# Kernel optimization log

Hardware: AMD Instinct MI355X
Metric: run time of the kernel (lower is better)

The kernel has to match this reference:

```python
import jax, jax.numpy as jnp
import numpy as np


def setup_inputs() -> dict:
    key = jax.random.key(0)
    k1, k2, k3 = jax.random.split(key, 3)
    B, H, L, D = 4, 16, 1024, 64
    q = jax.random.normal(k1, (B, H, L, D), dtype=jnp.float32)
    k = jax.random.normal(k2, (B, H, L, D), dtype=jnp.float32)
    attn_mask = jax.random.randint(k3, (B, H, L, L), 0, 2).astype(bool)
    return {"q": q, "k": k, "attn_mask": attn_mask}


def reference(q, k, attn_mask):
    # q, k: [B, H, L, D]. The original builds a [B,H,L,D,L] tensor
    # c[b,h,i,m,j] = exp(-(q[b,h,i,m]-k[b,h,j,m])^2), then for each dim m
    # keeps only the entries where rank of q[i,m] (along seq) equals rank of
    # k[j,m], scatters them into an LxL grid and averages over m.
    # Equivalent fused form: sort q and k per dimension, pair equal ranks,
    # and scatter-add exp(-(q_sorted - k_sorted)^2)/D into p[b,h,i,j].
    B, H, L, D = q.shape
    q_idx = jnp.argsort(q, axis=2)                       # [B,H,L,D] int
    k_idx = jnp.argsort(k, axis=2)
    q_sorted = jnp.take_along_axis(q, q_idx, axis=2)     # [B,H,L,D]
    k_sorted = jnp.take_along_axis(k, k_idx, axis=2)
    diff = q_sorted - k_sorted
    vals = jnp.exp(-(diff * diff))                       # [B,H,L,D]
    # linear index into the flattened [L,L] grid, plus batch*head offset
    lin = q_idx * L + k_idx                              # [B,H,L,D]
    bh_off = (jnp.arange(B * H) * (L * L)).reshape(B, H, 1, 1)
    flat_idx = (lin + bh_off).ravel()
    p = jnp.zeros(B * H * L * L, dtype=q.dtype).at[flat_idx].add(vals.ravel())
    p = (p / D).reshape(B, H, L, L)
    return jnp.where(attn_mask, jnp.zeros((), dtype=p.dtype), p)
```

## Files before the change

kernel.cpp:

```cpp
#include <hip/hip_runtime.h>
#include <stdint.h>
#include <string.h>


#define LL 1024
#define DD 64
#define NBH 64
#define PAIRS_BYTES ((size_t)NBH * DD * LL * 4)

typedef float    vf4   __attribute__((ext_vector_type(4)));
typedef uint32_t vu4   __attribute__((ext_vector_type(4)));
typedef int32_t  vi4   __attribute__((ext_vector_type(4)));
typedef unsigned long long vu64x2 __attribute__((ext_vector_type(2)));

__device__ __forceinline__ uint32_t f2ord(float x) {
    uint32_t u = __float_as_uint(x);
    return (u & 0x80000000u) ? ~u : (u | 0x80000000u);
}
__device__ __forceinline__ float ord2f(uint32_t o) {
    uint32_t u = (o & 0x80000000u) ? (o & 0x7fffffffu) : ~o;
    return __uint_as_float(u);
}

__global__ __launch_bounds__(256) void swd3_phase1(
    const float* __restrict__ q, const float* __restrict__ k,
    uint32_t* __restrict__ pairs)
{
    __shared__ alignas(16) uint64_t sq[LL];
    __shared__ alignas(16) uint64_t sk[LL];

    const int raw  = blockIdx.x;
    const int slot = raw >> 3;
    const int bh   = (raw & 7) * 8 + (slot >> 6);
    const int d    = slot & 63;
    const int t    = threadIdx.x;

    const size_t colbase = (size_t)bh * (LL * DD) + d;
    uint64_t xq[4], xk[4];
    #pragma unroll
    for (int s = 0; s < 4; ++s) {
        const uint32_t e = 4u * t + s;
        xq[s] = ((uint64_t)f2ord(q[colbase + (size_t)e * DD]) << 32) | e;
        xk[s] = ((uint64_t)f2ord(k[colbase + (size_t)e * DD]) << 32) | e;
    }

    auto cex = [](uint64_t& a, uint64_t& b, bool up) {
        const uint64_t lo = a < b ? a : b;
        const uint64_t hi = a < b ? b : a;
        a = up ? lo : hi; b = up ? hi : lo;
    };
    auto shfl64 = [&](uint64_t v, int m) -> uint64_t {
        const uint32_t lo = __shfl_xor((uint32_t)v, m);
        const uint32_t hi = __shfl_xor((uint32_t)(v >> 32), m);
        return ((uint64_t)hi << 32) | lo;
    };
    auto shfl_step = [&](int m, bool up) {
        const bool keepmin = (((t & m) == 0) == up);
        #pragma unroll
        for (int s = 0; s < 4; ++s) {
            uint64_t y = shfl64(xq[s], m);
            xq[s] = keepmin ? (xq[s] < y ? xq[s] : y) : (xq[s] > y ? xq[s] : y);
            y = shfl64(xk[s], m);
            xk[s] = keepmin ? (xk[s] < y ? xk[s] : y) : (xk[s] > y ? xk[s] : y);
        }
    };
    auto internal2 = [&](bool up) {
        cex(xq[0], xq[2], up); cex(xq[1], xq[3], up);
        cex(xk[0], xk[2], up); cex(xk[1], xk[3], up);
    };
    auto internal1 = [&](bool up) {
        cex(xq[0], xq[1], up); cex(xq[2], xq[3], up);
        cex(xk[0], xk[1], up); cex(xk[2], xk[3], up);
    };
    auto lds_step = [&](int j, int k2) {
        #pragma unroll
        for (int h = 0; h < 2; ++h) {
            const int v = t + h * 256;
            const int r = v & (j - 1);
            const int a = ((v ^ r) << 1) | r;
            const int b = a | j;
            const bool upl = ((a & k2) == 0);
            uint64_t xa = sq[a], xb = sq[b];
            if ((xa > xb) == upl) { sq[a] = xb; sq[b] = xa; }
            xa = sk[a]; xb = sk[b];
            if ((xa > xb) == upl) { sk[a] = xb; sk[b] = xa; }
        }
        __syncthreads();
    };
    auto store_regs = [&]() {
        vu64x2* q2 = (vu64x2*)sq;
        vu64x2* k2p = (vu64x2*)sk;
        vu64x2 v;
        v.x = xq[0]; v.y = xq[1]; q2[2 * t] = v;
        v.x = xq[2]; v.y = xq[3]; q2[2 * t + 1] = v;
        v.x = xk[0]; v.y = xk[1]; k2p[2 * t] = v;
        v.x = xk[2]; v.y = xk[3]; k2p[2 * t + 1] = v;
        __syncthreads();
    };
    auto load_regs = [&]() {
        const vu64x2* q2 = (const vu64x2*)sq;
        const vu64x2* k2p = (const vu64x2*)sk;
        vu64x2 v;
        v = q2[2 * t];     xq[0] = v.x; xq[1] = v.y;
        v = q2[2 * t + 1]; xq[2] = v.x; xq[3] = v.y;
        v = k2p[2 * t];     xk[0] = v.x; xk[1] = v.y;
        v = k2p[2 * t + 1]; xk[2] = v.x; xk[3] = v.y;
    };

    cex(xq[0], xq[1], true);  cex(xq[2], xq[3], false);
    cex(xk[0], xk[1], true);  cex(xk[2], xk[3], false);
    { const bool up = ((t & 1) == 0); internal2(up); internal1(up); }
    #pragma unroll
    for (int lk = 3; lk <= 8; ++lk) {
        const int k2 = 1 << lk;
        const bool up = ((t & (k2 >> 2)) == 0);
        #pragma unroll
        for (int m = k2 >> 3; m >= 1; m >>= 1) shfl_step(m, up);
        internal2(up); internal1(up);
    }
    {
        const bool up = ((t & 128) == 0);
        store_regs();
        lds_step(256, 512);
        load_regs();
        #pragma unroll
        for (int m = 32; m >= 1; m >>= 1) shfl_step(m, up);
        internal2(up); internal1(up);
    }
    {
        store_regs();
        lds_step(512, 1024);
        lds_step(256, 1024);
        load_regs();
        #pragma unroll
        for (int m = 32; m >= 1; m >>= 1) shfl_step(m, true);
        internal2(true); internal1(true);
    }

    __syncthreads();
    uint32_t* pr = (uint32_t*)sq;
    #pragma unroll
    for (int s = 0; s < 4; ++s) {
        const uint32_t iq = (uint32_t)xq[s] & 1023u;
        const uint32_t ik = (uint32_t)xk[s] & 1023u;
        const float df = ord2f((uint32_t)(xq[s] >> 32))
                       - ord2f((uint32_t)(xk[s] >> 32));
        const float val = __expf(-df * df) * (1.0f / 64.0f);
        pr[iq] = (__float_as_uint(val) & 0xFFFFFC00u) | ik;
    }
    __syncthreads();

    vu4* pp4 = (vu4*)(pairs + ((size_t)bh * DD + d) * LL);
    pp4[t] = ((const vu4*)pr)[t];
}

__global__ __launch_bounds__(256) void swd3_phase2(
    const uint32_t* __restrict__ pairs, const void* __restrict__ maskp,
    float* __restrict__ out)
{
    __shared__ alignas(16) float acc[8 * LL];
    __shared__ uint32_t sdet[4];

    const int bh = blockIdx.x >> 7;
    const int s  = blockIdx.x & 127;
    const int i0 = s * 8;
    const int t  = threadIdx.x;

    {
        const uint32_t w = ((const uint32_t*)maskp)[t];
        const uint64_t bal = __ballot(w > 1u);
        if ((t & 63) == 0) sdet[t >> 6] = (bal != 0ull) ? 1u : 0u;
    }

    vf4* acc4 = (vf4*)acc;
    #pragma unroll
    for (int v = 0; v < 8; ++v) {
        vf4 z; z.x = 0.f; z.y = 0.f; z.z = 0.f; z.w = 0.f;
        acc4[v * 256 + t] = z;
    }
    __syncthreads();

    const bool mask_byte =
        ((sdet[0] | sdet[1] | sdet[2] | sdet[3]) != 0u);
    const size_t cellbase = ((size_t)bh << 20) + ((size_t)i0 << 10);

    uint32_t mb[8];
    vi4      mi[8];
    if (mask_byte) {
        const uint32_t* mp = (const uint32_t*)maskp + (cellbase >> 2);
        #pragma unroll
        for (int v = 0; v < 8; ++v)
            mb[v] = __builtin_nontemporal_load(mp + v * 256 + t);
    } else {
        const vi4* mp = (const vi4*)((const int32_t*)maskp + cellbase);
        #pragma unroll
        for (int v = 0; v < 8; ++v)
            mi[v] = __builtin_nontemporal_load(mp + v * 256 + t);
    }

    {
        const uint32_t* pb = pairs + (size_t)bh * (DD * LL);
        const int dd = t >> 2;
        const uint2 pv = ((const uint2*)(pb + dd * LL + i0))[t & 3];
        const int ii0 = 2 * (t & 3), ii1 = ii0 + 1;
        atomicAdd(&acc[ii0 * LL + (int)(pv.x & 1023u)],
                  __uint_as_float(pv.x & 0xFFFFFC00u));
        atomicAdd(&acc[ii1 * LL + (int)(pv.y & 1023u)],
                  __uint_as_float(pv.y & 0xFFFFFC00u));
    }
    __syncthreads();

    vf4* ob = (vf4*)(out + cellbase);
    #pragma unroll
    for (int v = 0; v < 8; ++v) {
        const int p = v * 256 + t;
        const vf4 a = acc4[p];
        int mx, my, mz, mw2;
        if (mask_byte) {
            const uint32_t m = mb[v];
            mx = (int)(m & 0xFFu); my = (int)((m >> 8) & 0xFFu);
            mz = (int)((m >> 16) & 0xFFu); mw2 = (int)(m >> 24);
        } else {
            mx = mi[v].x; my = mi[v].y; mz = mi[v].z; mw2 = mi[v].w;
        }
        vf4 r;
        r.x = mx  ? 0.f : a.x;
        r.y = my  ? 0.f : a.y;
        r.z = mz  ? 0.f : a.z;
        r.w = mw2 ? 0.f : a.w;
        __builtin_nontemporal_store(r, ob + p);
    }
}

extern "C" void kernel_launch(void* const* d_in, const int* in_sizes, int n_in,
                              void* d_out, int out_size, void* d_ws, size_t ws_size,
                              hipStream_t stream) {
    const float* q = (const float*)d_in[0];
    const float* k = (const float*)d_in[1];
    const void* mask = d_in[2];
    uint32_t* pairs = (uint32_t*)d_ws;

    const bool ws_ok = (ws_size >= PAIRS_BYTES);
    hipError_t e1 = hipSuccess, e2 = hipSuccess;
    (void)hipGetLastError();

    if (ws_ok) {
        swd3_phase1<<<NBH * DD, 256, 0, stream>>>(q, k, pairs);
        e1 = hipGetLastError();
        swd3_phase2<<<NBH * 128, 256, 0, stream>>>(pairs, mask, (float*)d_out);
        e2 = hipGetLastError();
    }

    if (!ws_ok || e1 != hipSuccess || e2 != hipSuccess) {
        static float h_stamp[8];
        h_stamp[0] = !ws_ok ? (9000.0f + (float)(ws_size >> 20))
                            : (1000.0f + (float)(int)e1);
        h_stamp[1] = 2000.0f + (float)(int)e2;
        h_stamp[2] = h_stamp[0];
        h_stamp[3] = h_stamp[1];
        hipMemcpyAsync(d_out, h_stamp, sizeof(h_stamp),
                       hipMemcpyHostToDevice, stream);
    }
}
```

Before: 549.2 us.

## Sort each column within a single wavefront using registers and shuffles

Phase 1 now assigns one 1024-element column to each 64-lane wavefront, with 16 elements per lane, instead of one column per 256-thread block. The bitonic sort runs entirely in registers and cross-lane shuffles, so the LDS exchange steps and block-wide barriers go away. Each block handles four columns and the grid shrinks by four. The cost is a much higher register count, since 32 64-bit values are held per thread, which the launch bound of 3 blocks tries to contain and which may cause spills or lower occupancy.

```diff
diff --git a/kernel.cpp b/kernel.cpp
--- a/kernel.cpp
+++ b/kernel.cpp
@@ -11,7 +11,6 @@
 typedef float    vf4   __attribute__((ext_vector_type(4)));
 typedef uint32_t vu4   __attribute__((ext_vector_type(4)));
 typedef int32_t  vi4   __attribute__((ext_vector_type(4)));
-typedef unsigned long long vu64x2 __attribute__((ext_vector_type(2)));
 
 __device__ __forceinline__ uint32_t f2ord(float x) {
     uint32_t u = __float_as_uint(x);
@@ -22,24 +21,27 @@
     return __uint_as_float(u);
 }
 
-__global__ __launch_bounds__(256) void swd3_phase1(
+__global__ __launch_bounds__(256, 3) void swd3_phase1(
     const float* __restrict__ q, const float* __restrict__ k,
     uint32_t* __restrict__ pairs)
 {
-    __shared__ alignas(16) uint64_t sq[LL];
-    __shared__ alignas(16) uint64_t sk[LL];
+    __shared__ alignas(16) uint32_t pr[4][LL];
 
     const int raw  = blockIdx.x;
     const int slot = raw >> 3;
-    const int bh   = (raw & 7) * 8 + (slot >> 6);
-    const int d    = slot & 63;
+    const int bh   = (raw & 7) * 8 + (slot >> 4);
+    const int dg   = slot & 15;
     const int t    = threadIdx.x;
+    const int w    = t >> 6;
+    const int lane = t & 63;
+    const int d    = dg * 4 + w;
 
     const size_t colbase = (size_t)bh * (LL * DD) + d;
-    uint64_t xq[4], xk[4];
-    #pragma unroll
-    for (int s = 0; s < 4; ++s) {
-        const uint32_t e = 4u * t + s;
+
+    uint64_t xq[16], xk[16];
+    #pragma unroll
+    for (int s = 0; s < 16; ++s) {
+        const uint32_t e = 16u * (uint32_t)lane + (uint32_t)s;
         xq[s] = ((uint64_t)f2ord(q[colbase + (size_t)e * DD]) << 32) | e;
         xk[s] = ((uint64_t)f2ord(k[colbase + (size_t)e * DD]) << 32) | e;
     }
@@ -49,109 +51,78 @@
         const uint64_t hi = a < b ? b : a;
         a = up ? lo : hi; b = up ? hi : lo;
     };
-    auto shfl64 = [&](uint64_t v, int m) -> uint64_t {
+    auto shfl64 = [](uint64_t v, int m) -> uint64_t {
         const uint32_t lo = __shfl_xor((uint32_t)v, m);
         const uint32_t hi = __shfl_xor((uint32_t)(v >> 32), m);
         return ((uint64_t)hi << 32) | lo;
     };
     auto shfl_step = [&](int m, bool up) {
-        const bool keepmin = (((t & m) == 0) == up);
-        #pragma unroll
-        for (int s = 0; s < 4; ++s) {
+        const bool keepmin = (((lane & m) == 0) == up);
+        #pragma unroll
+        for (int s = 0; s < 16; ++s) {
             uint64_t y = shfl64(xq[s], m);
             xq[s] = keepmin ? (xq[s] < y ? xq[s] : y) : (xq[s] > y ? xq[s] : y);
             y = shfl64(xk[s], m);
             xk[s] = keepmin ? (xk[s] < y ? xk[s] : y) : (xk[s] > y ? xk[s] : y);
         }
     };
-    auto internal2 = [&](bool up) {
-        cex(xq[0], xq[2], up); cex(xq[1], xq[3], up);
-        cex(xk[0], xk[2], up); cex(xk[1], xk[3], up);
-    };
-    auto internal1 = [&](bool up) {
-        cex(xq[0], xq[1], up); cex(xq[2], xq[3], up);
-        cex(xk[0], xk[1], up); cex(xk[2], xk[3], up);
-    };
-    auto lds_step = [&](int j, int k2) {
-        #pragma unroll
-        for (int h = 0; h < 2; ++h) {
-            const int v = t + h * 256;
-            const int r = v & (j - 1);
-            const int a = ((v ^ r) << 1) | r;
-            const int b = a | j;
-            const bool upl = ((a & k2) == 0);
-            uint64_t xa = sq[a], xb = sq[b];
-            if ((xa > xb) == upl) { sq[a] = xb; sq[b] = xa; }
-            xa = sk[a]; xb = sk[b];
-            if ((xa > xb) == upl) { sk[a] = xb; sk[b] = xa; }
-        }
-        __syncthreads();
-    };
-    auto store_regs = [&]() {
-        vu64x2* q2 = (vu64x2*)sq;
-        vu64x2* k2p = (vu64x2*)sk;
-        vu64x2 v;
-        v.x = xq[0]; v.y = xq[1]; q2[2 * t] = v;
-        v.x = xq[2]; v.y = xq[3]; q2[2 * t + 1] = v;
-        v.x = xk[0]; v.y = xk[1]; k2p[2 * t] = v;
-        v.x = xk[2]; v.y = xk[3]; k2p[2 * t + 1] = v;
-        __syncthreads();
-    };
-    auto load_regs = [&]() {
-        const vu64x2* q2 = (const vu64x2*)sq;
-        const vu64x2* k2p = (const vu64x2*)sk;
-        vu64x2 v;
-        v = q2[2 * t];     xq[0] = v.x; xq[1] = v.y;
-        v = q2[2 * t + 1]; xq[2] = v.x; xq[3] = v.y;
-        v = k2p[2 * t];     xk[0] = v.x; xk[1] = v.y;
-        v = k2p[2 * t + 1]; xk[2] = v.x; xk[3] = v.y;
-    };
-
-    cex(xq[0], xq[1], true);  cex(xq[2], xq[3], false);
-    cex(xk[0], xk[1], true);  cex(xk[2], xk[3], false);
-    { const bool up = ((t & 1) == 0); internal2(up); internal1(up); }
-    #pragma unroll
-    for (int lk = 3; lk <= 8; ++lk) {
+
+    #pragma unroll
+    for (int lk = 1; lk <= 3; ++lk) {
         const int k2 = 1 << lk;
-        const bool up = ((t & (k2 >> 2)) == 0);
-        #pragma unroll
-        for (int m = k2 >> 3; m >= 1; m >>= 1) shfl_step(m, up);
-        internal2(up); internal1(up);
+        #pragma unroll
+        for (int j = k2 >> 1; j >= 1; j >>= 1) {
+            #pragma unroll
+            for (int s = 0; s < 16; ++s) {
+                if ((s & j) == 0) {
+                    const bool up = ((s & k2) == 0);
+                    cex(xq[s], xq[s | j], up);
+                    cex(xk[s], xk[s | j], up);
+                }
+            }
+        }
     }
     {
-        const bool up = ((t & 128) == 0);
-        store_regs();
-        lds_step(256, 512);
-        load_regs();
-        #pragma unroll
-        for (int m = 32; m >= 1; m >>= 1) shfl_step(m, up);
-        internal2(up); internal1(up);
-    }
-    {
-        store_regs();
-        lds_step(512, 1024);
-        lds_step(256, 1024);
-        load_regs();
-        #pragma unroll
-        for (int m = 32; m >= 1; m >>= 1) shfl_step(m, true);
-        internal2(true); internal1(true);
-    }
-
-    __syncthreads();
-    uint32_t* pr = (uint32_t*)sq;
-    #pragma unroll
-    for (int s = 0; s < 4; ++s) {
+        const bool up = ((lane & 1) == 0);
+        #pragma unroll
+        for (int j = 8; j >= 1; j >>= 1) {
+            #pragma unroll
+            for (int s = 0; s < 16; ++s)
+                if ((s & j) == 0) { cex(xq[s], xq[s | j], up);
+                                    cex(xk[s], xk[s | j], up); }
+        }
+    }
+    #pragma unroll
+    for (int lk = 5; lk <= 10; ++lk) {
+        const bool up = ((lane & (1 << (lk - 4))) == 0);
+        #pragma unroll
+        for (int m = 1 << (lk - 5); m >= 1; m >>= 1)
+            shfl_step(m, up);
+        #pragma unroll
+        for (int j = 8; j >= 1; j >>= 1) {
+            #pragma unroll
+            for (int s = 0; s < 16; ++s)
+                if ((s & j) == 0) { cex(xq[s], xq[s | j], up);
+                                    cex(xk[s], xk[s | j], up); }
+        }
+    }
+
+    uint32_t* prw = pr[w];
+    #pragma unroll
+    for (int s = 0; s < 16; ++s) {
         const uint32_t iq = (uint32_t)xq[s] & 1023u;
         const uint32_t ik = (uint32_t)xk[s] & 1023u;
         const float df = ord2f((uint32_t)(xq[s] >> 32))
                        - ord2f((uint32_t)(xk[s] >> 32));
         const float val = __expf(-df * df) * (1.0f / 64.0f);
-        pr[iq] = (__float_as_uint(val) & 0xFFFFFC00u) | ik;
-    }
-    __syncthreads();
-
+        prw[iq] = (__float_as_uint(val) & 0xFFFFFC00u) | ik;
+    }
+    __asm__ volatile("s_waitcnt lgkmcnt(0)" ::: "memory");
     vu4* pp4 = (vu4*)(pairs + ((size_t)bh * DD + d) * LL);
-    pp4[t] = ((const vu4*)pr)[t];
+    const vu4* src = (const vu4*)prw;
+    #pragma unroll
+    for (int r = 0; r < 4; ++r)
+        pp4[r * 64 + lane] = src[r * 64 + lane];
 }
 
 __global__ __launch_bounds__(256) void swd3_phase2(
@@ -245,7 +216,7 @@
     (void)hipGetLastError();
 
     if (ws_ok) {
-        swd3_phase1<<<NBH * DD, 256, 0, stream>>>(q, k, pairs);
+        swd3_phase1<<<NBH * DD / 4, 256, 0, stream>>>(q, k, pairs);
         e1 = hipGetLastError();
         swd3_phase2<<<NBH * 128, 256, 0, stream>>>(pairs, mask, (float*)d_out);
         e2 = hipGetLastError();
```

Result: no change. 555.4 us (+1.1%).
